# Performance work log

Hardware: AMD Instinct MI355X
Metric: run time of the kernel (lower is better)

The kernel has to match this reference:

```python
import jax, jax.numpy as jnp
import numpy as np

B, S, H, I, E, TOPK = 2, 2048, 1024, 2816, 7, 2


def setup_inputs() -> dict:
    key = jax.random.key(0)
    ks = jax.random.split(key, 8)
    sh = 1.0 / np.sqrt(H).astype(np.float32)   # fan-in scale for H->I projections
    si = 1.0 / np.sqrt(I).astype(np.float32)   # fan-in scale for I->H projections
    return {
        "x": jax.random.normal(ks[0], (B, S, H), jnp.float32),
        "Wg_shared": jax.random.normal(ks[1], (I, H), jnp.float32) * sh,
        "Wu_shared": jax.random.normal(ks[2], (I, H), jnp.float32) * sh,
        "Wd_shared": jax.random.normal(ks[3], (H, I), jnp.float32) * si,
        "Wg": jax.random.normal(ks[4], (E, I, H), jnp.float32) * sh,
        "Wu": jax.random.normal(ks[5], (E, I, H), jnp.float32) * sh,
        "Wd": jax.random.normal(ks[6], (E, H, I), jnp.float32) * si,
        "Wr": jax.random.normal(ks[7], (E, H), jnp.float32) * sh,
    }


def reference(x, Wg_shared, Wu_shared, Wd_shared, Wg, Wu, Wd, Wr):
    # Shared expert: SwiGLU MLP applied to every token.
    sg = jnp.einsum('bsh,ih->bsi', x, Wg_shared)
    su = jnp.einsum('bsh,ih->bsi', x, Wu_shared)
    shared_out = jnp.einsum('bsi,hi->bsh', jax.nn.silu(sg) * su, Wd_shared)

    # Router: top-k over logits, softmax over the selected k logits.
    router_logits = jnp.einsum('bsh,eh->bse', x, Wr)          # [B,S,E]
    rw, sel = jax.lax.top_k(router_logits, TOPK)              # [B,S,K]
    rw = jax.nn.softmax(rw, axis=-1)
    # Per-expert combine weight (equivalent to the scatter-built mask * weight).
    comb = jnp.sum(rw[..., None] * jax.nn.one_hot(sel, E, dtype=x.dtype), axis=2)  # [B,S,E]

    # Torch module runs every expert densely on every token, then masks.
    g = jnp.einsum('bsh,eih->ebsi', x, Wg)                    # [E,B,S,I]
    u = jnp.einsum('bsh,eih->ebsi', x, Wu)
    y = jnp.einsum('ebsi,ehi->ebsh', jax.nn.silu(g) * u, Wd)  # [E,B,S,H]
    moe_out = jnp.einsum('ebsh,bse->bsh', y, comb)

    return shared_out + moe_out, router_logits
```

## Files before the change

kernel.cpp:

```cpp
#include <hip/hip_runtime.h>
#include <hip/hip_bf16.h>

#define NTOK 4096
#define HH 1024
#define II 2816
#define EE 7
#define SHARED_BASE 8192
#define NSLOT 12288

typedef __bf16 bf16x8 __attribute__((ext_vector_type(8)));
typedef __bf16 bf16x4 __attribute__((ext_vector_type(4)));
typedef float  f32x4v __attribute__((ext_vector_type(4)));

__global__ void cvt_x(const float* __restrict__ x, __bf16* __restrict__ xb) {
    int i = blockIdx.x * blockDim.x + threadIdx.x;
    const f32x4v* xv = (const f32x4v*)x;
    bf16x4* ov = (bf16x4*)xb;
    int base = i * 4;
#pragma unroll
    for (int j = 0; j < 4; j++) {
        f32x4v f = xv[base + j];
        bf16x4 b;
        b[0] = (__bf16)f[0]; b[1] = (__bf16)f[1];
        b[2] = (__bf16)f[2]; b[3] = (__bf16)f[3];
        ov[base + j] = b;
    }
}

__global__ void router_k(const float* __restrict__ x, const float* __restrict__ Wr,
                         float* __restrict__ logits, int* __restrict__ counts,
                         int* __restrict__ sel, float* __restrict__ wtop,
                         int* __restrict__ tlist, float* __restrict__ wlist) {
    int wave = threadIdx.x >> 6;
    int lane = threadIdx.x & 63;
    int t = blockIdx.x * 4 + wave;
    const float* xr = x + (size_t)t * HH;
    double acc[EE];
#pragma unroll
    for (int e = 0; e < EE; e++) acc[e] = 0.0;
    for (int j = 0; j < 16; j++) {
        int h = lane + j * 64;
        double xv = (double)xr[h];
#pragma unroll
        for (int e = 0; e < EE; e++) acc[e] += xv * (double)Wr[e * HH + h];
    }
#pragma unroll
    for (int e = 0; e < EE; e++) {
        for (int off = 32; off > 0; off >>= 1) acc[e] += __shfl_down(acc[e], off, 64);
    }
    if (lane == 0) {
        int e0 = 0;
        for (int e = 1; e < EE; e++) if (acc[e] > acc[e0]) e0 = e;
        int e1 = -1;
        for (int e = 0; e < EE; e++) {
            if (e == e0) continue;
            if (e1 < 0 || acc[e] > acc[e1]) e1 = e;
        }
        double w1 = exp(acc[e1] - acc[e0]);
        double s = 1.0 + w1;
        for (int e = 0; e < EE; e++) logits[(size_t)t * EE + e] = (float)acc[e];
        sel[2 * t] = e0; sel[2 * t + 1] = e1;
        wtop[2 * t] = (float)(1.0 / s); wtop[2 * t + 1] = (float)(w1 / s);
        atomicAdd(&counts[e0], 1);
        atomicAdd(&counts[e1], 1);
        tlist[SHARED_BASE + t] = t;
        wlist[SHARED_BASE + t] = 1.0f;
    }
}

__global__ void finalize_k(const int* __restrict__ counts, int* __restrict__ cursor,
                           int* __restrict__ nlist, int* __restrict__ offs) {
    if (threadIdx.x == 0 && blockIdx.x == 0) {
        int o = 0;
        for (int e = 0; e < EE; e++) {
            offs[e] = o; cursor[e] = o; nlist[e] = counts[e];
            o += counts[e];
        }
        offs[EE] = SHARED_BASE;
        nlist[EE] = NTOK;
        cursor[EE] = SHARED_BASE;
    }
}

__global__ void scatter_k(const int* __restrict__ sel, const float* __restrict__ wtop,
                          int* __restrict__ cursor, int* __restrict__ tlist,
                          float* __restrict__ wlist) {
    int t = blockIdx.x * blockDim.x + threadIdx.x;
    if (t >= NTOK) return;
#pragma unroll
    for (int j = 0; j < 2; j++) {
        int e = sel[2 * t + j];
        int slot = atomicAdd(&cursor[e], 1);
        tlist[slot] = t;
        wlist[slot] = wtop[2 * t + j];
    }
}

__global__ __launch_bounds__(256, 3) void gateup_k(
        const float* __restrict__ Wg, const float* __restrict__ Wu,
        const float* __restrict__ Wgs, const float* __restrict__ Wus,
        const __bf16* __restrict__ xb, __bf16* __restrict__ hbuf,
        const int* __restrict__ nlist, const int* __restrict__ offs,
        const int* __restrict__ tlist) {
    const int e = blockIdx.z;
    const int ne = nlist[e];
    const int bx = blockIdx.x;
    const int nt = (bx & 7) + 8 * (bx >> 8);
    const int mt = (bx >> 3) & 31;
    if (nt >= II / 64) return;
    if (mt * 128 >= ne) return;
    const int base = offs[e];
    const float* wg = (e < EE) ? Wg + (size_t)e * II * HH : Wgs;
    const float* wu = (e < EE) ? Wu + (size_t)e * II * HH : Wus;

    __shared__ __bf16 As[128 * 32];
    __shared__ __bf16 Bg[64 * 32];
    __shared__ __bf16 Bu[64 * 32];

    const int tid = threadIdx.x;
    const int arow0 = tid >> 2, c8 = (tid & 3) * 8;
    const int arow1 = arow0 + 64;
    const int cl0 = min(mt * 128 + arow0, ne - 1);
    const int cl1 = min(mt * 128 + arow1, ne - 1);
    const __bf16* aptr0 = xb + (size_t)tlist[base + cl0] * HH + c8;
    const __bf16* aptr1 = xb + (size_t)tlist[base + cl1] * HH + c8;
    const int brow = tid >> 2;
    const size_t boff = (size_t)(nt * 64 + brow) * HH + c8;

    const int wid = tid >> 6, lane = tid & 63;
    const int wm = wid >> 1, wn = wid & 1;
    const int l16 = lane & 15, quad = lane >> 4;

    f32x4v accg[4][2], accu[4][2];
#pragma unroll
    for (int i = 0; i < 4; i++)
#pragma unroll
        for (int j = 0; j < 2; j++) { accg[i][j] = (f32x4v)0.0f; accu[i][j] = (f32x4v)0.0f; }

    bf16x8 aR0 = *(const bf16x8*)aptr0;
    bf16x8 aR1 = *(const bf16x8*)aptr1;
    f32x4v g0 = *(const f32x4v*)(wg + boff);
    f32x4v g1 = *(const f32x4v*)(wg + boff + 4);
    f32x4v u0 = *(const f32x4v*)(wu + boff);
    f32x4v u1 = *(const f32x4v*)(wu + boff + 4);

    for (int k0 = 0; k0 < HH; k0 += 32) {
        bf16x8 bgv, buv;
        bgv[0] = (__bf16)g0[0]; bgv[1] = (__bf16)g0[1]; bgv[2] = (__bf16)g0[2]; bgv[3] = (__bf16)g0[3];
        bgv[4] = (__bf16)g1[0]; bgv[5] = (__bf16)g1[1]; bgv[6] = (__bf16)g1[2]; bgv[7] = (__bf16)g1[3];
        buv[0] = (__bf16)u0[0]; buv[1] = (__bf16)u0[1]; buv[2] = (__bf16)u0[2]; buv[3] = (__bf16)u0[3];
        buv[4] = (__bf16)u1[0]; buv[5] = (__bf16)u1[1]; buv[6] = (__bf16)u1[2]; buv[7] = (__bf16)u1[3];
        __syncthreads();
        *(bf16x8*)&As[arow0 * 32 + c8] = aR0;
        *(bf16x8*)&As[arow1 * 32 + c8] = aR1;
        *(bf16x8*)&Bg[brow * 32 + c8] = bgv;
        *(bf16x8*)&Bu[brow * 32 + c8] = buv;
        if (k0 + 32 < HH) {
            aR0 = *(const bf16x8*)(aptr0 + k0 + 32);
            aR1 = *(const bf16x8*)(aptr1 + k0 + 32);
            g0 = *(const f32x4v*)(wg + boff + k0 + 32);
            g1 = *(const f32x4v*)(wg + boff + k0 + 36);
            u0 = *(const f32x4v*)(wu + boff + k0 + 32);
            u1 = *(const f32x4v*)(wu + boff + k0 + 36);
        }
        __syncthreads();
        bf16x8 a[4];
#pragma unroll
        for (int i = 0; i < 4; i++)
            a[i] = *(const bf16x8*)&As[(wm * 64 + i * 16 + l16) * 32 + quad * 8];
#pragma unroll
        for (int j = 0; j < 2; j++) {
            bf16x8 bg = *(const bf16x8*)&Bg[(wn * 32 + j * 16 + l16) * 32 + quad * 8];
            bf16x8 bu = *(const bf16x8*)&Bu[(wn * 32 + j * 16 + l16) * 32 + quad * 8];
#pragma unroll
            for (int i = 0; i < 4; i++) {
                accg[i][j] = __builtin_amdgcn_mfma_f32_16x16x32_bf16(a[i], bg, accg[i][j], 0, 0, 0);
                accu[i][j] = __builtin_amdgcn_mfma_f32_16x16x32_bf16(a[i], bu, accu[i][j], 0, 0, 0);
            }
        }
    }
#pragma unroll
    for (int i = 0; i < 4; i++) {
        const int mrow = mt * 128 + wm * 64 + i * 16 + quad * 4;
#pragma unroll
        for (int r = 0; r < 4; r++) {
            const int slot = mrow + r;
            if (slot < ne) {
                __bf16* hrow = hbuf + (size_t)(base + slot) * II + nt * 64 + wn * 32 + l16;
#pragma unroll
                for (int j = 0; j < 2; j++) {
                    float g = accg[i][j][r], u = accu[i][j][r];
                    float sgl = g / (1.0f + __expf(-g));
                    hrow[j * 16] = (__bf16)(sgl * u);
                }
            }
        }
    }
}

__global__ __launch_bounds__(256, 3) void down_k(
        const float* __restrict__ Wd, const float* __restrict__ Wds,
        const __bf16* __restrict__ hbuf, float* __restrict__ out,
        const int* __restrict__ nlist, const int* __restrict__ offs,
        const int* __restrict__ tlist, const float* __restrict__ wlist) {
    const int e = blockIdx.z;
    const int ne = nlist[e];
    const int bx = blockIdx.x;
    const int nt = bx & 7;
    const int mt = bx >> 3;
    if (mt * 128 >= ne) return;
    const int base = offs[e];
    const float* wd = (e < EE) ? Wd + (size_t)e * HH * II : Wds;

    __shared__ __bf16 As[128 * 32];
    __shared__ __bf16 Bs[128 * 32];

    const int tid = threadIdx.x;
    const int arow0 = tid >> 2, c8 = (tid & 3) * 8;
    const int arow1 = arow0 + 64;
    const int cl0 = min(mt * 128 + arow0, ne - 1);
    const int cl1 = min(mt * 128 + arow1, ne - 1);
    const __bf16* aptr0 = hbuf + (size_t)(base + cl0) * II + c8;
    const __bf16* aptr1 = hbuf + (size_t)(base + cl1) * II + c8;
    const size_t boff0 = (size_t)(nt * 128 + arow0) * II + c8;
    const size_t boff1 = (size_t)(nt * 128 + arow1) * II + c8;

    const int wid = tid >> 6, lane = tid & 63;
    const int wm = wid >> 1, wn = wid & 1;
    const int l16 = lane & 15, quad = lane >> 4;

    f32x4v acc[4][4];
#pragma unroll
    for (int i = 0; i < 4; i++)
#pragma unroll
        for (int j = 0; j < 4; j++) acc[i][j] = (f32x4v)0.0f;

    bf16x8 aR0 = *(const bf16x8*)aptr0;
    bf16x8 aR1 = *(const bf16x8*)aptr1;
    f32x4v b00 = *(const f32x4v*)(wd + boff0);
    f32x4v b01 = *(const f32x4v*)(wd + boff0 + 4);
    f32x4v b10 = *(const f32x4v*)(wd + boff1);
    f32x4v b11 = *(const f32x4v*)(wd + boff1 + 4);

    for (int k0 = 0; k0 < II; k0 += 32) {
        bf16x8 bs0, bs1;
        bs0[0] = (__bf16)b00[0]; bs0[1] = (__bf16)b00[1]; bs0[2] = (__bf16)b00[2]; bs0[3] = (__bf16)b00[3];
        bs0[4] = (__bf16)b01[0]; bs0[5] = (__bf16)b01[1]; bs0[6] = (__bf16)b01[2]; bs0[7] = (__bf16)b01[3];
        bs1[0] = (__bf16)b10[0]; bs1[1] = (__bf16)b10[1]; bs1[2] = (__bf16)b10[2]; bs1[3] = (__bf16)b10[3];
        bs1[4] = (__bf16)b11[0]; bs1[5] = (__bf16)b11[1]; bs1[6] = (__bf16)b11[2]; bs1[7] = (__bf16)b11[3];
        __syncthreads();
        *(bf16x8*)&As[arow0 * 32 + c8] = aR0;
        *(bf16x8*)&As[arow1 * 32 + c8] = aR1;
        *(bf16x8*)&Bs[arow0 * 32 + c8] = bs0;
        *(bf16x8*)&Bs[arow1 * 32 + c8] = bs1;
        if (k0 + 32 < II) {
            aR0 = *(const bf16x8*)(aptr0 + k0 + 32);
            aR1 = *(const bf16x8*)(aptr1 + k0 + 32);
            b00 = *(const f32x4v*)(wd + boff0 + k0 + 32);
            b01 = *(const f32x4v*)(wd + boff0 + k0 + 36);
            b10 = *(const f32x4v*)(wd + boff1 + k0 + 32);
            b11 = *(const f32x4v*)(wd + boff1 + k0 + 36);
        }
        __syncthreads();
        bf16x8 a[4];
#pragma unroll
        for (int i = 0; i < 4; i++)
            a[i] = *(const bf16x8*)&As[(wm * 64 + i * 16 + l16) * 32 + quad * 8];
#pragma unroll
        for (int j = 0; j < 4; j++) {
            bf16x8 b = *(const bf16x8*)&Bs[(wn * 64 + j * 16 + l16) * 32 + quad * 8];
#pragma unroll
            for (int i = 0; i < 4; i++)
                acc[i][j] = __builtin_amdgcn_mfma_f32_16x16x32_bf16(a[i], b, acc[i][j], 0, 0, 0);
        }
    }
#pragma unroll
    for (int i = 0; i < 4; i++) {
        const int mrow = mt * 128 + wm * 64 + i * 16 + quad * 4;
#pragma unroll
        for (int r = 0; r < 4; r++) {
            const int slot = mrow + r;
            if (slot < ne) {
                const int idx = base + slot;
                const int tok = tlist[idx];
                const float w = wlist[idx];
                float* orow = out + (size_t)tok * HH + nt * 128 + wn * 64 + l16;
#pragma unroll
                for (int j = 0; j < 4; j++)
                    atomicAdd(&orow[j * 16], w * acc[i][j][r]);
            }
        }
    }
}

extern "C" void kernel_launch(void* const* d_in, const int* in_sizes, int n_in,
                              void* d_out, int out_size, void* d_ws, size_t ws_size,
                              hipStream_t stream) {
    const float* x   = (const float*)d_in[0];
    const float* Wgs = (const float*)d_in[1];
    const float* Wus = (const float*)d_in[2];
    const float* Wds = (const float*)d_in[3];
    const float* Wg  = (const float*)d_in[4];
    const float* Wu  = (const float*)d_in[5];
    const float* Wd  = (const float*)d_in[6];
    const float* Wr  = (const float*)d_in[7];
    float* out = (float*)d_out;
    float* logits = out + (size_t)NTOK * HH;

    char* ws = (char*)d_ws;
    __bf16* hbuf = (__bf16*)ws;
    __bf16* xb   = (__bf16*)(ws + (size_t)NSLOT * II * 2);
    char* meta   = ws + (size_t)NSLOT * II * 2 + (size_t)NTOK * HH * 2;
    int* counts = (int*)meta;
    int* cursor = counts + 8;
    int* nlist  = cursor + 8;
    int* offs   = nlist + 8;
    int* sel    = offs + 8;
    int* tlist  = sel + 2 * NTOK;
    float* wtop = (float*)(tlist + NSLOT);
    float* wlist = wtop + 2 * NTOK;

    hipMemsetAsync(counts, 0, 8 * sizeof(int), stream);
    hipMemsetAsync(out, 0, (size_t)NTOK * HH * sizeof(float), stream);

    cvt_x<<<1024, 256, 0, stream>>>(x, xb);
    router_k<<<NTOK / 4, 256, 0, stream>>>(x, Wr, logits, counts, sel, wtop, tlist, wlist);
    finalize_k<<<1, 64, 0, stream>>>(counts, cursor, nlist, offs);
    scatter_k<<<NTOK / 256, 256, 0, stream>>>(sel, wtop, cursor, tlist, wlist);
    gateup_k<<<dim3(1536, 1, EE + 1), 256, 0, stream>>>(Wg, Wu, Wgs, Wus, xb, hbuf,
                                                        nlist, offs, tlist);
    down_k<<<dim3(256, 1, EE + 1), 256, 0, stream>>>(Wd, Wds, hbuf, out,
                                                     nlist, offs, tlist, wlist);
}
```

Baseline: 821.0 us.

## Pre-convert weights to bf16, use direct global-to-LDS loads, replace atomics with combine

Adds a kernel that converts all expert and shared weights to bf16 once per call, interleaving gate and up rows in blocks of 16 so one GEMM tile computes both. The GEMMs then use global_load_lds with an XOR-swizzled LDS layout instead of register staging with in-loop fp32->bf16 conversion. The down projection writes weighted per-slot outputs to a buffer, and a separate combine kernel sums the two routed slots and the shared slot per token. This removes the fp32 atomics and the output memset. In exchange, each call pays a full fp32 weight read plus a bf16 write, and the GEMM main loop loses its register prefetch, leaving a single-buffered load-sync-compute loop.

```diff
diff --git a/kernel.cpp b/kernel.cpp
--- a/kernel.cpp
+++ b/kernel.cpp
@@ -12,6 +12,12 @@
 typedef __bf16 bf16x4 __attribute__((ext_vector_type(4)));
 typedef float  f32x4v __attribute__((ext_vector_type(4)));
 
+typedef const __attribute__((address_space(1))) void* gas_ptr;
+typedef __attribute__((address_space(3))) void* las_ptr;
+__device__ __forceinline__ void load16_lds(const void* g, void* l) {
+    __builtin_amdgcn_global_load_lds((gas_ptr)g, (las_ptr)l, 16, 0, 0);
+}
+
 __global__ void cvt_x(const float* __restrict__ x, __bf16* __restrict__ xb) {
     int i = blockIdx.x * blockDim.x + threadIdx.x;
     const f32x4v* xv = (const f32x4v*)x;
@@ -24,6 +30,58 @@
         b[0] = (__bf16)f[0]; b[1] = (__bf16)f[1];
         b[2] = (__bf16)f[2]; b[3] = (__bf16)f[3];
         ov[base + j] = b;
+    }
+}
+
+__global__ void cvt_w6(const float* __restrict__ Wg, const float* __restrict__ Wu,
+                       const float* __restrict__ Wgs, const float* __restrict__ Wus,
+                       const float* __restrict__ Wd, const float* __restrict__ Wds,
+                       __bf16* __restrict__ wgu, __bf16* __restrict__ wgus,
+                       __bf16* __restrict__ wdb, __bf16* __restrict__ wdsb) {
+    const int y = blockIdx.y;
+    const int H4 = HH / 4;
+    const int stride = gridDim.x * blockDim.x;
+    int idx0 = blockIdx.x * blockDim.x + threadIdx.x;
+    if (y < 2) {
+        const f32x4v* sv = (const f32x4v*)(y == 0 ? Wg : Wu);
+        const int add = y * 16;
+        const int n4 = EE * II * H4;
+        for (int idx = idx0; idx < n4; idx += stride) {
+            int h4 = idx & (H4 - 1);
+            int row = idx >> 8;
+            int e = row / II, i = row - e * II;
+            int crow = e * 2 * II + ((i >> 4) * 32) + (i & 15) + add;
+            f32x4v f = sv[idx];
+            bf16x4 b;
+            b[0] = (__bf16)f[0]; b[1] = (__bf16)f[1];
+            b[2] = (__bf16)f[2]; b[3] = (__bf16)f[3];
+            ((bf16x4*)wgu)[crow * H4 + h4] = b;
+        }
+    } else if (y < 4) {
+        const f32x4v* sv = (const f32x4v*)(y == 2 ? Wgs : Wus);
+        const int add = (y - 2) * 16;
+        const int n4 = II * H4;
+        for (int idx = idx0; idx < n4; idx += stride) {
+            int h4 = idx & (H4 - 1);
+            int i = idx >> 8;
+            int crow = ((i >> 4) * 32) + (i & 15) + add;
+            f32x4v f = sv[idx];
+            bf16x4 b;
+            b[0] = (__bf16)f[0]; b[1] = (__bf16)f[1];
+            b[2] = (__bf16)f[2]; b[3] = (__bf16)f[3];
+            ((bf16x4*)wgus)[crow * H4 + h4] = b;
+        }
+    } else {
+        const f32x4v* sv = (const f32x4v*)(y == 4 ? Wd : Wds);
+        bf16x4* dv = (bf16x4*)(y == 4 ? wdb : wdsb);
+        const int n4 = (y == 4 ? EE : 1) * HH * II / 4;
+        for (int idx = idx0; idx < n4; idx += stride) {
+            f32x4v f = sv[idx];
+            bf16x4 b;
+            b[0] = (__bf16)f[0]; b[1] = (__bf16)f[1];
+            b[2] = (__bf16)f[2]; b[3] = (__bf16)f[3];
+            dv[idx] = b;
+        }
     }
 }
 
@@ -84,7 +142,7 @@
 
 __global__ void scatter_k(const int* __restrict__ sel, const float* __restrict__ wtop,
                           int* __restrict__ cursor, int* __restrict__ tlist,
-                          float* __restrict__ wlist) {
+                          float* __restrict__ wlist, int* __restrict__ inv) {
     int t = blockIdx.x * blockDim.x + threadIdx.x;
     if (t >= NTOK) return;
 #pragma unroll
@@ -93,12 +151,12 @@
         int slot = atomicAdd(&cursor[e], 1);
         tlist[slot] = t;
         wlist[slot] = wtop[2 * t + j];
-    }
-}
-
-__global__ __launch_bounds__(256, 3) void gateup_k(
-        const float* __restrict__ Wg, const float* __restrict__ Wu,
-        const float* __restrict__ Wgs, const float* __restrict__ Wus,
+        inv[2 * t + j] = slot;
+    }
+}
+
+__global__ __launch_bounds__(256, 3) void gateup_gu(
+        const __bf16* __restrict__ Wgu, const __bf16* __restrict__ Wgus,
         const __bf16* __restrict__ xb, __bf16* __restrict__ hbuf,
         const int* __restrict__ nlist, const int* __restrict__ offs,
         const int* __restrict__ tlist) {
@@ -107,76 +165,57 @@
     const int bx = blockIdx.x;
     const int nt = (bx & 7) + 8 * (bx >> 8);
     const int mt = (bx >> 3) & 31;
-    if (nt >= II / 64) return;
+    if (nt >= (2 * II) / 128) return;
     if (mt * 128 >= ne) return;
     const int base = offs[e];
-    const float* wg = (e < EE) ? Wg + (size_t)e * II * HH : Wgs;
-    const float* wu = (e < EE) ? Wu + (size_t)e * II * HH : Wus;
+    const __bf16* w = (e < EE) ? Wgu + (size_t)e * 2 * II * HH : Wgus;
 
     __shared__ __bf16 As[128 * 32];
-    __shared__ __bf16 Bg[64 * 32];
-    __shared__ __bf16 Bu[64 * 32];
+    __shared__ __bf16 Bs[128 * 32];
 
     const int tid = threadIdx.x;
-    const int arow0 = tid >> 2, c8 = (tid & 3) * 8;
-    const int arow1 = arow0 + 64;
-    const int cl0 = min(mt * 128 + arow0, ne - 1);
-    const int cl1 = min(mt * 128 + arow1, ne - 1);
-    const __bf16* aptr0 = xb + (size_t)tlist[base + cl0] * HH + c8;
-    const __bf16* aptr1 = xb + (size_t)tlist[base + cl1] * HH + c8;
-    const int brow = tid >> 2;
-    const size_t boff = (size_t)(nt * 64 + brow) * HH + c8;
+    const int r0 = tid >> 2;
+    const int c  = tid & 3;
+    const int cs = (c ^ ((r0 >> 1) & 3)) * 8;
+    const int cl0 = min(mt * 128 + r0, ne - 1);
+    const int cl1 = min(mt * 128 + r0 + 64, ne - 1);
+    const __bf16* aptr0 = xb + (size_t)tlist[base + cl0] * HH + cs;
+    const __bf16* aptr1 = xb + (size_t)tlist[base + cl1] * HH + cs;
+    const __bf16* bptr0 = w + (size_t)(nt * 128 + r0) * HH + cs;
+    const __bf16* bptr1 = w + (size_t)(nt * 128 + r0 + 64) * HH + cs;
+    __bf16* ldsA0 = &As[tid * 8];
+    __bf16* ldsA1 = &As[64 * 32 + tid * 8];
+    __bf16* ldsB0 = &Bs[tid * 8];
+    __bf16* ldsB1 = &Bs[64 * 32 + tid * 8];
 
     const int wid = tid >> 6, lane = tid & 63;
     const int wm = wid >> 1, wn = wid & 1;
     const int l16 = lane & 15, quad = lane >> 4;
-
-    f32x4v accg[4][2], accu[4][2];
+    const int qsw = (quad ^ ((l16 >> 1) & 3)) * 8;
+
+    f32x4v acc[4][4];
 #pragma unroll
     for (int i = 0; i < 4; i++)
 #pragma unroll
-        for (int j = 0; j < 2; j++) { accg[i][j] = (f32x4v)0.0f; accu[i][j] = (f32x4v)0.0f; }
-
-    bf16x8 aR0 = *(const bf16x8*)aptr0;
-    bf16x8 aR1 = *(const bf16x8*)aptr1;
-    f32x4v g0 = *(const f32x4v*)(wg + boff);
-    f32x4v g1 = *(const f32x4v*)(wg + boff + 4);
-    f32x4v u0 = *(const f32x4v*)(wu + boff);
-    f32x4v u1 = *(const f32x4v*)(wu + boff + 4);
+        for (int j = 0; j < 4; j++) acc[i][j] = (f32x4v)0.0f;
 
     for (int k0 = 0; k0 < HH; k0 += 32) {
-        bf16x8 bgv, buv;
-        bgv[0] = (__bf16)g0[0]; bgv[1] = (__bf16)g0[1]; bgv[2] = (__bf16)g0[2]; bgv[3] = (__bf16)g0[3];
-        bgv[4] = (__bf16)g1[0]; bgv[5] = (__bf16)g1[1]; bgv[6] = (__bf16)g1[2]; bgv[7] = (__bf16)g1[3];
-        buv[0] = (__bf16)u0[0]; buv[1] = (__bf16)u0[1]; buv[2] = (__bf16)u0[2]; buv[3] = (__bf16)u0[3];
-        buv[4] = (__bf16)u1[0]; buv[5] = (__bf16)u1[1]; buv[6] = (__bf16)u1[2]; buv[7] = (__bf16)u1[3];
         __syncthreads();
-        *(bf16x8*)&As[arow0 * 32 + c8] = aR0;
-        *(bf16x8*)&As[arow1 * 32 + c8] = aR1;
-        *(bf16x8*)&Bg[brow * 32 + c8] = bgv;
-        *(bf16x8*)&Bu[brow * 32 + c8] = buv;
-        if (k0 + 32 < HH) {
-            aR0 = *(const bf16x8*)(aptr0 + k0 + 32);
-            aR1 = *(const bf16x8*)(aptr1 + k0 + 32);
-            g0 = *(const f32x4v*)(wg + boff + k0 + 32);
-            g1 = *(const f32x4v*)(wg + boff + k0 + 36);
-            u0 = *(const f32x4v*)(wu + boff + k0 + 32);
-            u1 = *(const f32x4v*)(wu + boff + k0 + 36);
-        }
+        load16_lds(aptr0 + k0, ldsA0);
+        load16_lds(aptr1 + k0, ldsA1);
+        load16_lds(bptr0 + k0, ldsB0);
+        load16_lds(bptr1 + k0, ldsB1);
         __syncthreads();
         bf16x8 a[4];
 #pragma unroll
         for (int i = 0; i < 4; i++)
-            a[i] = *(const bf16x8*)&As[(wm * 64 + i * 16 + l16) * 32 + quad * 8];
-#pragma unroll
-        for (int j = 0; j < 2; j++) {
-            bf16x8 bg = *(const bf16x8*)&Bg[(wn * 32 + j * 16 + l16) * 32 + quad * 8];
-            bf16x8 bu = *(const bf16x8*)&Bu[(wn * 32 + j * 16 + l16) * 32 + quad * 8];
-#pragma unroll
-            for (int i = 0; i < 4; i++) {
-                accg[i][j] = __builtin_amdgcn_mfma_f32_16x16x32_bf16(a[i], bg, accg[i][j], 0, 0, 0);
-                accu[i][j] = __builtin_amdgcn_mfma_f32_16x16x32_bf16(a[i], bu, accu[i][j], 0, 0, 0);
-            }
+            a[i] = *(const bf16x8*)&As[(wm * 64 + i * 16 + l16) * 32 + qsw];
+#pragma unroll
+        for (int j = 0; j < 4; j++) {
+            bf16x8 b = *(const bf16x8*)&Bs[(wn * 64 + j * 16 + l16) * 32 + qsw];
+#pragma unroll
+            for (int i = 0; i < 4; i++)
+                acc[i][j] = __builtin_amdgcn_mfma_f32_16x16x32_bf16(a[i], b, acc[i][j], 0, 0, 0);
         }
     }
 #pragma unroll
@@ -188,19 +227,19 @@
             if (slot < ne) {
                 __bf16* hrow = hbuf + (size_t)(base + slot) * II + nt * 64 + wn * 32 + l16;
 #pragma unroll
-                for (int j = 0; j < 2; j++) {
-                    float g = accg[i][j][r], u = accu[i][j][r];
+                for (int jj = 0; jj < 2; jj++) {
+                    float g = acc[i][2 * jj][r], u = acc[i][2 * jj + 1][r];
                     float sgl = g / (1.0f + __expf(-g));
-                    hrow[j * 16] = (__bf16)(sgl * u);
+                    hrow[jj * 16] = (__bf16)(sgl * u);
                 }
             }
         }
     }
 }
 
-__global__ __launch_bounds__(256, 3) void down_k(
-        const float* __restrict__ Wd, const float* __restrict__ Wds,
-        const __bf16* __restrict__ hbuf, float* __restrict__ out,
+__global__ __launch_bounds__(256, 3) void down_y(
+        const __bf16* __restrict__ Wd, const __bf16* __restrict__ Wds,
+        const __bf16* __restrict__ hbuf, float* __restrict__ ybuf,
         const int* __restrict__ nlist, const int* __restrict__ offs,
         const int* __restrict__ tlist, const float* __restrict__ wlist) {
     const int e = blockIdx.z;
@@ -210,24 +249,30 @@
     const int mt = bx >> 3;
     if (mt * 128 >= ne) return;
     const int base = offs[e];
-    const float* wd = (e < EE) ? Wd + (size_t)e * HH * II : Wds;
+    const __bf16* wd = (e < EE) ? Wd + (size_t)e * HH * II : Wds;
 
     __shared__ __bf16 As[128 * 32];
     __shared__ __bf16 Bs[128 * 32];
 
     const int tid = threadIdx.x;
-    const int arow0 = tid >> 2, c8 = (tid & 3) * 8;
-    const int arow1 = arow0 + 64;
-    const int cl0 = min(mt * 128 + arow0, ne - 1);
-    const int cl1 = min(mt * 128 + arow1, ne - 1);
-    const __bf16* aptr0 = hbuf + (size_t)(base + cl0) * II + c8;
-    const __bf16* aptr1 = hbuf + (size_t)(base + cl1) * II + c8;
-    const size_t boff0 = (size_t)(nt * 128 + arow0) * II + c8;
-    const size_t boff1 = (size_t)(nt * 128 + arow1) * II + c8;
+    const int r0 = tid >> 2;
+    const int c  = tid & 3;
+    const int cs = (c ^ ((r0 >> 1) & 3)) * 8;
+    const int cl0 = min(mt * 128 + r0, ne - 1);
+    const int cl1 = min(mt * 128 + r0 + 64, ne - 1);
+    const __bf16* aptr0 = hbuf + (size_t)(base + cl0) * II + cs;
+    const __bf16* aptr1 = hbuf + (size_t)(base + cl1) * II + cs;
+    const __bf16* bptr0 = wd + (size_t)(nt * 128 + r0) * II + cs;
+    const __bf16* bptr1 = wd + (size_t)(nt * 128 + r0 + 64) * II + cs;
+    __bf16* ldsA0 = &As[tid * 8];
+    __bf16* ldsA1 = &As[64 * 32 + tid * 8];
+    __bf16* ldsB0 = &Bs[tid * 8];
+    __bf16* ldsB1 = &Bs[64 * 32 + tid * 8];
 
     const int wid = tid >> 6, lane = tid & 63;
     const int wm = wid >> 1, wn = wid & 1;
     const int l16 = lane & 15, quad = lane >> 4;
+    const int qsw = (quad ^ ((l16 >> 1) & 3)) * 8;
 
     f32x4v acc[4][4];
 #pragma unroll
@@ -235,40 +280,20 @@
 #pragma unroll
         for (int j = 0; j < 4; j++) acc[i][j] = (f32x4v)0.0f;
 
-    bf16x8 aR0 = *(const bf16x8*)aptr0;
-    bf16x8 aR1 = *(const bf16x8*)aptr1;
-    f32x4v b00 = *(const f32x4v*)(wd + boff0);
-    f32x4v b01 = *(const f32x4v*)(wd + boff0 + 4);
-    f32x4v b10 = *(const f32x4v*)(wd + boff1);
-    f32x4v b11 = *(const f32x4v*)(wd + boff1 + 4);
-
     for (int k0 = 0; k0 < II; k0 += 32) {
-        bf16x8 bs0, bs1;
-        bs0[0] = (__bf16)b00[0]; bs0[1] = (__bf16)b00[1]; bs0[2] = (__bf16)b00[2]; bs0[3] = (__bf16)b00[3];
-        bs0[4] = (__bf16)b01[0]; bs0[5] = (__bf16)b01[1]; bs0[6] = (__bf16)b01[2]; bs0[7] = (__bf16)b01[3];
-        bs1[0] = (__bf16)b10[0]; bs1[1] = (__bf16)b10[1]; bs1[2] = (__bf16)b10[2]; bs1[3] = (__bf16)b10[3];
-        bs1[4] = (__bf16)b11[0]; bs1[5] = (__bf16)b11[1]; bs1[6] = (__bf16)b11[2]; bs1[7] = (__bf16)b11[3];
         __syncthreads();
-        *(bf16x8*)&As[arow0 * 32 + c8] = aR0;
-        *(bf16x8*)&As[arow1 * 32 + c8] = aR1;
-        *(bf16x8*)&Bs[arow0 * 32 + c8] = bs0;
-        *(bf16x8*)&Bs[arow1 * 32 + c8] = bs1;
-        if (k0 + 32 < II) {
-            aR0 = *(const bf16x8*)(aptr0 + k0 + 32);
-            aR1 = *(const bf16x8*)(aptr1 + k0 + 32);
-            b00 = *(const f32x4v*)(wd + boff0 + k0 + 32);
-            b01 = *(const f32x4v*)(wd + boff0 + k0 + 36);
-            b10 = *(const f32x4v*)(wd + boff1 + k0 + 32);
-            b11 = *(const f32x4v*)(wd + boff1 + k0 + 36);
-        }
+        load16_lds(aptr0 + k0, ldsA0);
+        load16_lds(aptr1 + k0, ldsA1);
+        load16_lds(bptr0 + k0, ldsB0);
+        load16_lds(bptr1 + k0, ldsB1);
         __syncthreads();
         bf16x8 a[4];
 #pragma unroll
         for (int i = 0; i < 4; i++)
-            a[i] = *(const bf16x8*)&As[(wm * 64 + i * 16 + l16) * 32 + quad * 8];
+            a[i] = *(const bf16x8*)&As[(wm * 64 + i * 16 + l16) * 32 + qsw];
 #pragma unroll
         for (int j = 0; j < 4; j++) {
-            bf16x8 b = *(const bf16x8*)&Bs[(wn * 64 + j * 16 + l16) * 32 + quad * 8];
+            bf16x8 b = *(const bf16x8*)&Bs[(wn * 64 + j * 16 + l16) * 32 + qsw];
 #pragma unroll
             for (int i = 0; i < 4; i++)
                 acc[i][j] = __builtin_amdgcn_mfma_f32_16x16x32_bf16(a[i], b, acc[i][j], 0, 0, 0);
@@ -282,15 +307,25 @@
             const int slot = mrow + r;
             if (slot < ne) {
                 const int idx = base + slot;
-                const int tok = tlist[idx];
                 const float w = wlist[idx];
-                float* orow = out + (size_t)tok * HH + nt * 128 + wn * 64 + l16;
+                float* orow = ybuf + (size_t)idx * HH + nt * 128 + wn * 64 + l16;
 #pragma unroll
                 for (int j = 0; j < 4; j++)
-                    atomicAdd(&orow[j * 16], w * acc[i][j][r]);
+                    orow[j * 16] = w * acc[i][j][r];
             }
         }
     }
+}
+
+__global__ void combine_k(const float* __restrict__ ybuf, const int* __restrict__ inv,
+                          float* __restrict__ out) {
+    int idx = blockIdx.x * blockDim.x + threadIdx.x;
+    int t = idx >> 8, h4 = idx & 255;
+    const f32x4v* y0 = (const f32x4v*)(ybuf + (size_t)inv[2 * t] * HH);
+    const f32x4v* y1 = (const f32x4v*)(ybuf + (size_t)inv[2 * t + 1] * HH);
+    const f32x4v* ys = (const f32x4v*)(ybuf + (size_t)(SHARED_BASE + t) * HH);
+    f32x4v r = y0[h4] + y1[h4] + ys[h4];
+    ((f32x4v*)(out + (size_t)t * HH))[h4] = r;
 }
 
 extern "C" void kernel_launch(void* const* d_in, const int* in_sizes, int n_in,
@@ -307,10 +342,20 @@
     float* out = (float*)d_out;
     float* logits = out + (size_t)NTOK * HH;
 
+    const size_t HB  = (size_t)NSLOT * II * 2;
+    const size_t XB  = (size_t)NTOK * HH * 2;
+    const size_t WEB = (size_t)EE * II * HH * 2;
+    const size_t WSB = (size_t)II * HH * 2;
+
     char* ws = (char*)d_ws;
     __bf16* hbuf = (__bf16*)ws;
-    __bf16* xb   = (__bf16*)(ws + (size_t)NSLOT * II * 2);
-    char* meta   = ws + (size_t)NSLOT * II * 2 + (size_t)NTOK * HH * 2;
+    __bf16* xb   = (__bf16*)(ws + HB);
+    __bf16* wgu  = (__bf16*)(ws + HB + XB);
+    float*  ybuf = (float*)wgu;
+    __bf16* wdb  = (__bf16*)(ws + HB + XB + 2 * WEB);
+    __bf16* wgus = (__bf16*)(ws + HB + XB + 3 * WEB);
+    __bf16* wdsb = (__bf16*)(ws + HB + XB + 3 * WEB + 2 * WSB);
+    char* meta   = ws + HB + XB + 3 * WEB + 3 * WSB;
     int* counts = (int*)meta;
     int* cursor = counts + 8;
     int* nlist  = cursor + 8;
@@ -319,16 +364,19 @@
     int* tlist  = sel + 2 * NTOK;
     float* wtop = (float*)(tlist + NSLOT);
     float* wlist = wtop + 2 * NTOK;
+    int* inv    = (int*)(wlist + NSLOT);
 
     hipMemsetAsync(counts, 0, 8 * sizeof(int), stream);
-    hipMemsetAsync(out, 0, (size_t)NTOK * HH * sizeof(float), stream);
 
     cvt_x<<<1024, 256, 0, stream>>>(x, xb);
+    cvt_w6<<<dim3(1024, 6), 256, 0, stream>>>(Wg, Wu, Wgs, Wus, Wd, Wds,
+                                              wgu, wgus, wdb, wdsb);
     router_k<<<NTOK / 4, 256, 0, stream>>>(x, Wr, logits, counts, sel, wtop, tlist, wlist);
     finalize_k<<<1, 64, 0, stream>>>(counts, cursor, nlist, offs);
-    scatter_k<<<NTOK / 256, 256, 0, stream>>>(sel, wtop, cursor, tlist, wlist);
-    gateup_k<<<dim3(1536, 1, EE + 1), 256, 0, stream>>>(Wg, Wu, Wgs, Wus, xb, hbuf,
-                                                        nlist, offs, tlist);
-    down_k<<<dim3(256, 1, EE + 1), 256, 0, stream>>>(Wd, Wds, hbuf, out,
+    scatter_k<<<NTOK / 256, 256, 0, stream>>>(sel, wtop, cursor, tlist, wlist, inv);
+    gateup_gu<<<dim3(1536, 1, EE + 1), 256, 0, stream>>>(wgu, wgus, xb, hbuf,
+                                                         nlist, offs, tlist);
+    down_y<<<dim3(256, 1, EE + 1), 256, 0, stream>>>(wdb, wdsb, hbuf, ybuf,
                                                      nlist, offs, tlist, wlist);
-}
+    combine_k<<<NTOK, 256, 0, stream>>>(ybuf, inv, out);
+}
```

Result: faster. 770.9 us (-6.1%).
